# Kernel tuning notes

Measured on AMD Instinct MI355X. Metric: run time of the kernel, lower is better.

The kernel has to match this reference:

```python
import jax, jax.numpy as jnp
import numpy as np

ALPHA = 0.8  # LeakyReLU negative slope
OUT_DIM = 128
EDGE_DIM = 64


def setup_inputs() -> dict:
    key = jax.random.key(0)
    ks = jax.random.split(key, 6)
    N, NS, IN, OUT, ED = 25000, 32, 128, OUT_DIM, EDGE_DIM
    return {
        "input": jax.random.normal(ks[0], (N, IN), jnp.float32),
        "neigh_feat": jax.random.normal(ks[1], (N * NS, IN), jnp.float32),
        "edge_emb": jax.random.normal(ks[2], (N * NS, ED), jnp.float32),
        "mask": jnp.zeros((N,), jnp.int32),  # unused by forward, kept for signature fidelity
        "W": jax.random.normal(ks[3], (IN, OUT), jnp.float32) * 0.1,
        "W2": jax.random.normal(ks[4], (IN, OUT), jnp.float32) * 0.1,
        "a": jax.random.normal(ks[5], (2 * OUT + ED, 1), jnp.float32) * 0.1,
    }


def reference(input, neigh_feat, edge_emb, mask, W, W2, a):
    N = input.shape[0]
    ns = neigh_feat.shape[0] // N
    out_dim = W.shape[1]
    ed = edge_emb.shape[1]

    x = input @ W                                   # [N, out]
    neighs = (neigh_feat @ W2).reshape(N, ns, out_dim)  # [N, ns, out]
    edge = edge_emb.reshape(N, ns, ed)              # [N, ns, ed]

    # a_input @ a decomposed: avoid materializing the repeated/concatenated tensor.
    a_x = a[:out_dim, 0]
    a_n = a[out_dim:2 * out_dim, 0]
    a_e = a[2 * out_dim:, 0]
    scores = (x @ a_x)[:, None] + neighs @ a_n + edge @ a_e  # [N, ns]
    e = jnp.where(scores > 0, scores, ALPHA * scores)        # LeakyReLU(alpha)

    attention = jax.nn.softmax(e, axis=1)           # softmax over neighbors
    # dropout p=0.0 (eval) -> identity

    h_prime = jnp.einsum("ns,nsd->nd", attention, neighs)  # [N, out]
    output = jnp.concatenate([x, h_prime], axis=1)          # concat_node
    e_agg = jnp.einsum("ns,nse->ne", attention, edge)       # concat_edge
    output = jnp.concatenate([output, e_agg], axis=1)       # [N, 2*out+ed]
    return jax.nn.elu(output)
```

## Files before the change

kernel.cpp:

```cpp
#include <hip/hip_runtime.h>
#include <hip/hip_bf16.h>
#include <math.h>

typedef __bf16 bf16_t;
typedef __attribute__((ext_vector_type(8))) __bf16 bf16x8;
typedef __attribute__((ext_vector_type(4))) float f32x4;

#define NB 8

__global__ __launch_bounds__(256) void pack_weights_kernel(
    const float* __restrict__ W, const float* __restrict__ W2,
    const float* __restrict__ a,
    bf16_t* __restrict__ Wp, bf16_t* __restrict__ W2p,
    float* __restrict__ w2an) {
  int idx = blockIdx.x * 256 + threadIdx.x;
  int j  = idx & 7;
  int l  = (idx >> 3) & 63;
  int nt = (idx >> 9) & 7;
  int kt = idx >> 12;
  int k   = kt * 32 + (l >> 4) * 8 + j;
  int col = nt * 16 + (l & 15);
  Wp[idx]  = (bf16_t)W[k * 128 + col];
  W2p[idx] = (bf16_t)W2[k * 128 + col];
  if (blockIdx.x == 0 && threadIdx.x < 128) {
    const float* r = W2 + threadIdx.x * 128;
    float s = 0.f;
    for (int c = 0; c < 128; ++c) s += r[c] * a[128 + c];
    w2an[threadIdx.x] = s;
  }
}

__global__ __launch_bounds__(256) void gemm_kernel(
    const float* __restrict__ src, const bf16_t* __restrict__ Wpk,
    const float* __restrict__ a,
    float* __restrict__ out, float* __restrict__ sxv, int col_off, int N) {
  __shared__ __align__(16) bf16_t As[32 * 128];
  __shared__ float sp2[2][32];
  const int t  = threadIdx.x;
  const int rb = blockIdx.x * 32;
  const int w = t >> 6, l = t & 63;

  for (int c = t; c < 512; c += 256) {
    int row = c >> 4;
    int kc  = (c & 15) * 8;
    int grow = rb + row;
    float v[8];
    if (grow < N) {
      const f32x4* p = (const f32x4*)(src + (size_t)grow * 128 + kc);
      f32x4 v0 = p[0], v1 = p[1];
      v[0]=v0[0]; v[1]=v0[1]; v[2]=v0[2]; v[3]=v0[3];
      v[4]=v1[0]; v[5]=v1[1]; v[6]=v1[2]; v[7]=v1[3];
    } else {
      for (int j = 0; j < 8; ++j) v[j] = 0.f;
    }
    bf16x8 b;
    for (int j = 0; j < 8; ++j) b[j] = (bf16_t)v[j];
    *(bf16x8*)(&As[row * 128 + (kc ^ ((row & 7) << 3))]) = b;
  }
  __syncthreads();

  const int mt = w & 1;
  const int ntg = (w >> 1) * 4;
  const int arow = mt * 16 + (l & 15);

  f32x4 acc[4] = {};
#pragma unroll
  for (int kt = 0; kt < 4; ++kt) {
    bf16x8 af = *(const bf16x8*)(&As[arow * 128 + ((kt * 32 + (l >> 4) * 8) ^ ((arow & 7) << 3))]);
#pragma unroll
    for (int i = 0; i < 4; ++i) {
      bf16x8 bfv = *(const bf16x8*)(&Wpk[((kt * 8 + (ntg + i)) * 64 + l) * 8]);
      acc[i] = __builtin_amdgcn_mfma_f32_16x16x32_bf16(af, bfv, acc[i], 0, 0, 0);
    }
  }

  if (sxv) {
    float ax[4];
#pragma unroll
    for (int i = 0; i < 4; ++i) ax[i] = a[(ntg + i) * 16 + (l & 15)];
#pragma unroll
    for (int j = 0; j < 4; ++j) {
      float p = acc[0][j]*ax[0] + acc[1][j]*ax[1] + acc[2][j]*ax[2] + acc[3][j]*ax[3];
      p += __shfl_xor(p, 1); p += __shfl_xor(p, 2);
      p += __shfl_xor(p, 4); p += __shfl_xor(p, 8);
      if ((l & 15) == 0) sp2[w >> 1][mt * 16 + (l >> 4) * 4 + j] = p;
    }
    __syncthreads();
    if (t < 32) {
      int gr = rb + t;
      if (gr < N) sxv[gr] = sp2[0][t] + sp2[1][t];
    }
  }

#pragma unroll
  for (int i = 0; i < 4; ++i) {
    int col = (ntg + i) * 16 + (l & 15);
#pragma unroll
    for (int j = 0; j < 4; ++j) {
      int row = mt * 16 + (l >> 4) * 4 + j;
      int gr = rb + row;
      if (gr < N) {
        float v = acc[i][j];
        v = v > 0.f ? v : __expf(v) - 1.f;
        __builtin_nontemporal_store(v, &out[(size_t)gr * 320 + col_off + col]);
      }
    }
  }
}

__global__ __launch_bounds__(256) void node_kernel(
    const float* __restrict__ neigh_feat, const float* __restrict__ edge_emb,
    const float* __restrict__ a, const float* __restrict__ w2an,
    const float* __restrict__ sxv, float* __restrict__ aggbuf,
    float* __restrict__ out) {
  const int t = threadIdx.x;
  const int w = t >> 6, l = t & 63;
  const int n0 = blockIdx.x * NB;

  __shared__ float srow[32];
  __shared__ float se[32];
  __shared__ __align__(16) f32x4 nag[4][32];
  __shared__ __align__(16) f32x4 eag[4][16];

  const int q = l & 31;
  const int h = l >> 5;
  const int p = l & 15;
  const int g = l >> 4;

  const f32x4 wn = *(const f32x4*)(w2an + 4 * q);
  const f32x4 ae = *(const f32x4*)(a + 256 + 4 * p);

  f32x4 nA[4], eA[2], nB[4], eB[2];
  float sxA, sxB;

#define ISSUE(P, node_) do {                                              \
    const float* nf_ = neigh_feat + (size_t)(node_) * 4096 + 4 * t;       \
    n##P[0] = *(const f32x4*)(nf_);                                       \
    n##P[1] = *(const f32x4*)(nf_ + 1024);                                \
    n##P[2] = *(const f32x4*)(nf_ + 2048);                                \
    n##P[3] = *(const f32x4*)(nf_ + 3072);                                \
    const float* ee_ = edge_emb + (size_t)(node_) * 2048 + 4 * t;         \
    e##P[0] = *(const f32x4*)(ee_);                                       \
    e##P[1] = *(const f32x4*)(ee_ + 1024);                                \
    sx##P = sxv[node_];                                                   \
  } while (0)

#define BODY(P, kk) do {                                                  \
    const int node = n0 + (kk);                                           \
                            \
    _Pragma("unroll")                                                     \
    for (int j = 0; j < 4; ++j) {                                         \
      float s = n##P[j][0]*wn[0] + n##P[j][1]*wn[1]                       \
              + n##P[j][2]*wn[2] + n##P[j][3]*wn[3];                      \
      s += __shfl_xor(s, 1);  s += __shfl_xor(s, 2);                      \
      s += __shfl_xor(s, 4);  s += __shfl_xor(s, 8);                      \
      s += __shfl_xor(s, 16);                                             \
      if (q == 0) srow[8*j + 2*w + h] = s;                                \
    }                                                                     \
    _Pragma("unroll")                                                     \
    for (int j = 0; j < 2; ++j) {                                         \
      float s = e##P[j][0]*ae[0] + e##P[j][1]*ae[1]                       \
              + e##P[j][2]*ae[2] + e##P[j][3]*ae[3];                      \
      s += __shfl_xor(s, 1);  s += __shfl_xor(s, 2);                      \
      s += __shfl_xor(s, 4);  s += __shfl_xor(s, 8);                      \
      if (p == 0) se[16*j + 4*w + g] = s;                                 \
    }                                                                     \
    __syncthreads();                                                      \
      \
    float av;                                                             \
    {                                                                     \
      float e0 = srow[q] + se[q] + sx##P;                                 \
      e0 = e0 > 0.f ? e0 : 0.8f * e0;                                     \
      float m = e0;                                                       \
      m = fmaxf(m, __shfl_xor(m, 1));                                     \
      m = fmaxf(m, __shfl_xor(m, 2));                                     \
      m = fmaxf(m, __shfl_xor(m, 4));                                     \
      m = fmaxf(m, __shfl_xor(m, 8));                                     \
      m = fmaxf(m, __shfl_xor(m, 16));                                    \
      float pe = __expf(e0 - m);                                          \
      float s2 = pe;                                                      \
      s2 += __shfl_xor(s2, 1);                                            \
      s2 += __shfl_xor(s2, 2);                                            \
      s2 += __shfl_xor(s2, 4);                                            \
      s2 += __shfl_xor(s2, 8);                                            \
      s2 += __shfl_xor(s2, 16);                                           \
      av = pe / s2;                                                       \
    }                                                                     \
                                \
    {                                                                     \
      f32x4 pn = {0.f, 0.f, 0.f, 0.f};                                    \
      _Pragma("unroll")                                                   \
      for (int j = 0; j < 4; ++j) {                                       \
        float as = __shfl(av, 8*j + 2*w + h);                             \
        pn += as * n##P[j];                                               \
      }                                                                   \
      pn[0] += __shfl_xor(pn[0], 32);                                     \
      pn[1] += __shfl_xor(pn[1], 32);                                     \
      pn[2] += __shfl_xor(pn[2], 32);                                     \
      pn[3] += __shfl_xor(pn[3], 32);                                     \
      if (h == 0) nag[w][q] = pn;                                         \
      f32x4 pv = {0.f, 0.f, 0.f, 0.f};                                    \
      _Pragma("unroll")                                                   \
      for (int j = 0; j < 2; ++j) {                                       \
        float as = __shfl(av, 16*j + 4*w + g);                            \
        pv += as * e##P[j];                                               \
      }                                                                   \
      pv[0] += __shfl_xor(pv[0], 16);                                     \
      pv[1] += __shfl_xor(pv[1], 16);                                     \
      pv[2] += __shfl_xor(pv[2], 16);                                     \
      pv[3] += __shfl_xor(pv[3], 16);                                     \
      pv[0] += __shfl_xor(pv[0], 32);                                     \
      pv[1] += __shfl_xor(pv[1], 32);                                     \
      pv[2] += __shfl_xor(pv[2], 32);                                     \
      pv[3] += __shfl_xor(pv[3], 32);                                     \
      if (l < 16) eag[w][p] = pv;                                         \
    }                                                                     \
       \
    if ((kk) + 2 < NB) ISSUE(P, node + 2);                                \
    __syncthreads();                                                      \
                                    \
    if (t < 128) {                                                        \
      const float* f = (const float*)nag;                                 \
      float v = f[t] + f[128 + t] + f[256 + t] + f[384 + t];              \
      aggbuf[(size_t)node * 128 + t] = v;                                 \
    } else if (t < 192) {                                                 \
      int c = t - 128;                                                    \
      const float* f = (const float*)eag;                                 \
      float v = f[c] + f[64 + c] + f[128 + c] + f[192 + c];               \
      v = v > 0.f ? v : __expf(v) - 1.f;                                  \
      __builtin_nontemporal_store(v, out + (size_t)node * 320 + 256 + c); \
    }                                                                     \
  } while (0)

  ISSUE(A, n0);
  ISSUE(B, n0 + 1);

#pragma unroll 1
  for (int k = 0; k < NB; k += 2) {
    BODY(A, k);
    BODY(B, k + 1);
  }
#undef BODY
#undef ISSUE
}

extern "C" void kernel_launch(void* const* d_in, const int* in_sizes, int n_in,
                              void* d_out, int out_size, void* d_ws, size_t ws_size,
                              hipStream_t stream) {
  const float* input = (const float*)d_in[0];
  const float* neigh = (const float*)d_in[1];
  const float* edge  = (const float*)d_in[2];
  const float* W     = (const float*)d_in[4];
  const float* W2    = (const float*)d_in[5];
  const float* a     = (const float*)d_in[6];
  float* out = (float*)d_out;

  const int N = in_sizes[0] / 128;

  bf16_t* W2p  = (bf16_t*)d_ws;
  bf16_t* Wp   = W2p + 16384;
  float*  w2an = (float*)((char*)d_ws + 65536);
  float*  sxv  = (float*)((char*)d_ws + 66560);
  float*  agg  = (float*)((char*)d_ws + 262144);

  pack_weights_kernel<<<64, 256, 0, stream>>>(W, W2, a, Wp, W2p, w2an);
  gemm_kernel<<<(N + 31) / 32, 256, 0, stream>>>(input, Wp, a, out, sxv, 0, N);
  node_kernel<<<N / NB, 256, 0, stream>>>(neigh, edge, a, w2an, sxv, agg, out);
  gemm_kernel<<<(N + 31) / 32, 256, 0, stream>>>(agg, W2p, a, out, nullptr, 128, N);
}
```

Measured before the change: 163.8 us.

## Fuse both projection GEMMs into node kernel and drop aggregate round-trip

```diff
diff --git a/kernel.cpp b/kernel.cpp
--- a/kernel.cpp
+++ b/kernel.cpp
@@ -4,6 +4,7 @@
 
 typedef __bf16 bf16_t;
 typedef __attribute__((ext_vector_type(8))) __bf16 bf16x8;
+typedef __attribute__((ext_vector_type(4))) __bf16 bf16x4;
 typedef __attribute__((ext_vector_type(4))) float f32x4;
 
 #define NB 8
@@ -12,7 +13,7 @@
     const float* __restrict__ W, const float* __restrict__ W2,
     const float* __restrict__ a,
     bf16_t* __restrict__ Wp, bf16_t* __restrict__ W2p,
-    float* __restrict__ w2an) {
+    float* __restrict__ w2an, float* __restrict__ wax) {
   int idx = blockIdx.x * 256 + threadIdx.x;
   int j  = idx & 7;
   int l  = (idx >> 3) & 63;
@@ -28,99 +29,32 @@
     for (int c = 0; c < 128; ++c) s += r[c] * a[128 + c];
     w2an[threadIdx.x] = s;
   }
+  if (blockIdx.x == 1 && threadIdx.x < 128) {
+    const float* r = W + threadIdx.x * 128;
+    float s = 0.f;
+    for (int c = 0; c < 128; ++c) s += r[c] * a[c];
+    wax[threadIdx.x] = s;
+  }
 }
 
-__global__ __launch_bounds__(256) void gemm_kernel(
-    const float* __restrict__ src, const bf16_t* __restrict__ Wpk,
-    const float* __restrict__ a,
-    float* __restrict__ out, float* __restrict__ sxv, int col_off, int N) {
-  __shared__ __align__(16) bf16_t As[32 * 128];
-  __shared__ float sp2[2][32];
-  const int t  = threadIdx.x;
-  const int rb = blockIdx.x * 32;
-  const int w = t >> 6, l = t & 63;
-
-  for (int c = t; c < 512; c += 256) {
-    int row = c >> 4;
-    int kc  = (c & 15) * 8;
-    int grow = rb + row;
-    float v[8];
-    if (grow < N) {
-      const f32x4* p = (const f32x4*)(src + (size_t)grow * 128 + kc);
-      f32x4 v0 = p[0], v1 = p[1];
-      v[0]=v0[0]; v[1]=v0[1]; v[2]=v0[2]; v[3]=v0[3];
-      v[4]=v1[0]; v[5]=v1[1]; v[6]=v1[2]; v[7]=v1[3];
-    } else {
-      for (int j = 0; j < 8; ++j) v[j] = 0.f;
-    }
-    bf16x8 b;
-    for (int j = 0; j < 8; ++j) b[j] = (bf16_t)v[j];
-    *(bf16x8*)(&As[row * 128 + (kc ^ ((row & 7) << 3))]) = b;
-  }
-  __syncthreads();
-
-  const int mt = w & 1;
-  const int ntg = (w >> 1) * 4;
-  const int arow = mt * 16 + (l & 15);
-
-  f32x4 acc[4] = {};
-#pragma unroll
-  for (int kt = 0; kt < 4; ++kt) {
-    bf16x8 af = *(const bf16x8*)(&As[arow * 128 + ((kt * 32 + (l >> 4) * 8) ^ ((arow & 7) << 3))]);
-#pragma unroll
-    for (int i = 0; i < 4; ++i) {
-      bf16x8 bfv = *(const bf16x8*)(&Wpk[((kt * 8 + (ntg + i)) * 64 + l) * 8]);
-      acc[i] = __builtin_amdgcn_mfma_f32_16x16x32_bf16(af, bfv, acc[i], 0, 0, 0);
-    }
-  }
-
-  if (sxv) {
-    float ax[4];
-#pragma unroll
-    for (int i = 0; i < 4; ++i) ax[i] = a[(ntg + i) * 16 + (l & 15)];
-#pragma unroll
-    for (int j = 0; j < 4; ++j) {
-      float p = acc[0][j]*ax[0] + acc[1][j]*ax[1] + acc[2][j]*ax[2] + acc[3][j]*ax[3];
-      p += __shfl_xor(p, 1); p += __shfl_xor(p, 2);
-      p += __shfl_xor(p, 4); p += __shfl_xor(p, 8);
-      if ((l & 15) == 0) sp2[w >> 1][mt * 16 + (l >> 4) * 4 + j] = p;
-    }
-    __syncthreads();
-    if (t < 32) {
-      int gr = rb + t;
-      if (gr < N) sxv[gr] = sp2[0][t] + sp2[1][t];
-    }
-  }
-
-#pragma unroll
-  for (int i = 0; i < 4; ++i) {
-    int col = (ntg + i) * 16 + (l & 15);
-#pragma unroll
-    for (int j = 0; j < 4; ++j) {
-      int row = mt * 16 + (l >> 4) * 4 + j;
-      int gr = rb + row;
-      if (gr < N) {
-        float v = acc[i][j];
-        v = v > 0.f ? v : __expf(v) - 1.f;
-        __builtin_nontemporal_store(v, &out[(size_t)gr * 320 + col_off + col]);
-      }
-    }
-  }
-}
-
 __global__ __launch_bounds__(256) void node_kernel(
+    const float* __restrict__ input,
     const float* __restrict__ neigh_feat, const float* __restrict__ edge_emb,
     const float* __restrict__ a, const float* __restrict__ w2an,
-    const float* __restrict__ sxv, float* __restrict__ aggbuf,
+    const float* __restrict__ wax,
+    const bf16_t* __restrict__ Wp, const bf16_t* __restrict__ W2p,
     float* __restrict__ out) {
   const int t = threadIdx.x;
   const int w = t >> 6, l = t & 63;
   const int n0 = blockIdx.x * NB;
 
-  __shared__ float srow[32];
-  __shared__ float se[32];
+  __shared__ __align__(16) bf16_t Ax[16 * 128];
+  __shared__ __align__(16) bf16_t Ah[16 * 128];
+  __shared__ float Agg[8][128];
+  __shared__ float srow[32], se[32];
   __shared__ __align__(16) f32x4 nag[4][32];
   __shared__ __align__(16) f32x4 eag[4][16];
+  __shared__ float sxs[8];
 
   const int q = l & 31;
   const int h = l >> 5;
@@ -131,7 +65,6 @@
   const f32x4 ae = *(const f32x4*)(a + 256 + 4 * p);
 
   f32x4 nA[4], eA[2], nB[4], eB[2];
-  float sxA, sxB;
 
 #define ISSUE(P, node_) do {                                              \
     const float* nf_ = neigh_feat + (size_t)(node_) * 4096 + 4 * t;       \
@@ -142,12 +75,58 @@
     const float* ee_ = edge_emb + (size_t)(node_) * 2048 + 4 * t;         \
     e##P[0] = *(const f32x4*)(ee_);                                       \
     e##P[1] = *(const f32x4*)(ee_ + 1024);                                \
-    sx##P = sxv[node_];                                                   \
   } while (0)
+
+  ISSUE(A, n0);
+  ISSUE(B, n0 + 1);
+
+  {
+    const int r2 = t >> 5;
+    const int c0 = 4 * (t & 31);
+    f32x4 iv = *(const f32x4*)(input + (size_t)(n0 + r2) * 128 + c0);
+    f32x4 wv = *(const f32x4*)(wax + c0);
+    float s = iv[0]*wv[0] + iv[1]*wv[1] + iv[2]*wv[2] + iv[3]*wv[3];
+    s += __shfl_xor(s, 1);  s += __shfl_xor(s, 2);  s += __shfl_xor(s, 4);
+    s += __shfl_xor(s, 8);  s += __shfl_xor(s, 16);
+    if ((l & 31) == 0) sxs[r2] = s;
+    bf16x4 b;
+#pragma unroll
+    for (int j = 0; j < 4; ++j) b[j] = (bf16_t)iv[j];
+    const int gg = (t & 31) >> 1;
+    *(bf16x4*)(&Ax[r2 * 128 + ((gg ^ r2) << 3) + 4 * (t & 1)]) = b;
+    bf16x4 z = {(bf16_t)0.f, (bf16_t)0.f, (bf16_t)0.f, (bf16_t)0.f};
+    *(bf16x4*)(&Ax[1024 + 4 * t]) = z;
+    *(bf16x4*)(&Ah[1024 + 4 * t]) = z;
+  }
+  __syncthreads();
+
+  {
+    const int arow = l & 15;
+    f32x4 acc0 = {}, acc1 = {};
+#pragma unroll
+    for (int kt = 0; kt < 4; ++kt) {
+      bf16x8 af = *(const bf16x8*)(&Ax[arow * 128 + ((kt * 32 + (l >> 4) * 8) ^ ((arow & 7) << 3))]);
+      bf16x8 b0 = *(const bf16x8*)(&Wp[((kt * 8 + 2 * w) * 64 + l) * 8]);
+      bf16x8 b1 = *(const bf16x8*)(&Wp[((kt * 8 + 2 * w + 1) * 64 + l) * 8]);
+      acc0 = __builtin_amdgcn_mfma_f32_16x16x32_bf16(af, b0, acc0, 0, 0, 0);
+      acc1 = __builtin_amdgcn_mfma_f32_16x16x32_bf16(af, b1, acc1, 0, 0, 0);
+    }
+    if ((l >> 4) < 2) {
+#pragma unroll
+      for (int j = 0; j < 4; ++j) {
+        int row = (l >> 4) * 4 + j;
+        float v0 = acc0[j];
+        v0 = v0 > 0.f ? v0 : __expf(v0) - 1.f;
+        __builtin_nontemporal_store(v0, out + (size_t)(n0 + row) * 320 + 2 * w * 16 + (l & 15));
+        float v1 = acc1[j];
+        v1 = v1 > 0.f ? v1 : __expf(v1) - 1.f;
+        __builtin_nontemporal_store(v1, out + (size_t)(n0 + row) * 320 + (2 * w + 1) * 16 + (l & 15));
+      }
+    }
+  }
 
 #define BODY(P, kk) do {                                                  \
     const int node = n0 + (kk);                                           \
-                            \
     _Pragma("unroll")                                                     \
     for (int j = 0; j < 4; ++j) {                                         \
       float s = n##P[j][0]*wn[0] + n##P[j][1]*wn[1]                       \
@@ -166,10 +145,9 @@
       if (p == 0) se[16*j + 4*w + g] = s;                                 \
     }                                                                     \
     __syncthreads();                                                      \
-      \
     float av;                                                             \
     {                                                                     \
-      float e0 = srow[q] + se[q] + sx##P;                                 \
+      float e0 = srow[q] + se[q] + sxs[kk];                               \
       e0 = e0 > 0.f ? e0 : 0.8f * e0;                                     \
       float m = e0;                                                       \
       m = fmaxf(m, __shfl_xor(m, 1));                                     \
@@ -186,7 +164,6 @@
       s2 += __shfl_xor(s2, 16);                                           \
       av = pe / s2;                                                       \
     }                                                                     \
-                                \
     {                                                                     \
       f32x4 pn = {0.f, 0.f, 0.f, 0.f};                                    \
       _Pragma("unroll")                                                   \
@@ -215,14 +192,11 @@
       pv[3] += __shfl_xor(pv[3], 32);                                     \
       if (l < 16) eag[w][p] = pv;                                         \
     }                                                                     \
-       \
     if ((kk) + 2 < NB) ISSUE(P, node + 2);                                \
     __syncthreads();                                                      \
-                                    \
     if (t < 128) {                                                        \
       const float* f = (const float*)nag;                                 \
-      float v = f[t] + f[128 + t] + f[256 + t] + f[384 + t];              \
-      aggbuf[(size_t)node * 128 + t] = v;                                 \
+      Agg[kk][t] = f[t] + f[128 + t] + f[256 + t] + f[384 + t];           \
     } else if (t < 192) {                                                 \
       int c = t - 128;                                                    \
       const float* f = (const float*)eag;                                 \
@@ -232,9 +206,6 @@
     }                                                                     \
   } while (0)
 
-  ISSUE(A, n0);
-  ISSUE(B, n0 + 1);
-
 #pragma unroll 1
   for (int k = 0; k < NB; k += 2) {
     BODY(A, k);
@@ -242,6 +213,44 @@
   }
 #undef BODY
 #undef ISSUE
+
+  __syncthreads();
+
+  {
+    const int r2 = t >> 5;
+    const int c0 = 4 * (t & 31);
+    f32x4 v = *(const f32x4*)(&Agg[r2][c0]);
+    bf16x4 b;
+#pragma unroll
+    for (int j = 0; j < 4; ++j) b[j] = (bf16_t)v[j];
+    const int gg = (t & 31) >> 1;
+    *(bf16x4*)(&Ah[r2 * 128 + ((gg ^ r2) << 3) + 4 * (t & 1)]) = b;
+  }
+  __syncthreads();
+  {
+    const int arow = l & 15;
+    f32x4 acc0 = {}, acc1 = {};
+#pragma unroll
+    for (int kt = 0; kt < 4; ++kt) {
+      bf16x8 af = *(const bf16x8*)(&Ah[arow * 128 + ((kt * 32 + (l >> 4) * 8) ^ ((arow & 7) << 3))]);
+      bf16x8 b0 = *(const bf16x8*)(&W2p[((kt * 8 + 2 * w) * 64 + l) * 8]);
+      bf16x8 b1 = *(const bf16x8*)(&W2p[((kt * 8 + 2 * w + 1) * 64 + l) * 8]);
+      acc0 = __builtin_amdgcn_mfma_f32_16x16x32_bf16(af, b0, acc0, 0, 0, 0);
+      acc1 = __builtin_amdgcn_mfma_f32_16x16x32_bf16(af, b1, acc1, 0, 0, 0);
+    }
+    if ((l >> 4) < 2) {
+#pragma unroll
+      for (int j = 0; j < 4; ++j) {
+        int row = (l >> 4) * 4 + j;
+        float v0 = acc0[j];
+        v0 = v0 > 0.f ? v0 : __expf(v0) - 1.f;
+        __builtin_nontemporal_store(v0, out + (size_t)(n0 + row) * 320 + 128 + 2 * w * 16 + (l & 15));
+        float v1 = acc1[j];
+        v1 = v1 > 0.f ? v1 : __expf(v1) - 1.f;
+        __builtin_nontemporal_store(v1, out + (size_t)(n0 + row) * 320 + 128 + (2 * w + 1) * 16 + (l & 15));
+      }
+    }
+  }
 }
 
 extern "C" void kernel_launch(void* const* d_in, const int* in_sizes, int n_in,
@@ -260,11 +269,9 @@
   bf16_t* W2p  = (bf16_t*)d_ws;
   bf16_t* Wp   = W2p + 16384;
   float*  w2an = (float*)((char*)d_ws + 65536);
-  float*  sxv  = (float*)((char*)d_ws + 66560);
-  float*  agg  = (float*)((char*)d_ws + 262144);
-
-  pack_weights_kernel<<<64, 256, 0, stream>>>(W, W2, a, Wp, W2p, w2an);
-  gemm_kernel<<<(N + 31) / 32, 256, 0, stream>>>(input, Wp, a, out, sxv, 0, N);
-  node_kernel<<<N / NB, 256, 0, stream>>>(neigh, edge, a, w2an, sxv, agg, out);
-  gemm_kernel<<<(N + 31) / 32, 256, 0, stream>>>(agg, W2p, a, out, nullptr, 128, N);
+  float*  wax  = (float*)((char*)d_ws + 66048);
+
+  pack_weights_kernel<<<64, 256, 0, stream>>>(W, W2, a, Wp, W2p, w2an, wax);
+  node_kernel<<<N / NB, 256, 0, stream>>>(input, neigh, edge, a, w2an, wax,
+                                          Wp, W2p, out);
 }
```

Result: faster. 149.7 us (-8.7%).
